# Optimization experiments

Measured on AMD Instinct MI355X. Metric: run time of the kernel, lower is better.

## Reference

```python
import jax, jax.numpy as jnp
import numpy as np

HIDDEN = 1024
HEADS = 16
DEPTH = HIDDEN // HEADS  # 64
B, F, T = 2, 2048, 2048


def setup_inputs() -> dict:
    key = jax.random.key(0)
    ks = jax.random.split(key, 7)
    return {
        "query_input": jax.random.normal(ks[0], (B, F, HIDDEN), dtype=jnp.float32),
        "source_input": jax.random.normal(ks[1], (B, T, HIDDEN), dtype=jnp.float32),
        "bias": jax.random.normal(ks[2], (1, 1, F, T), dtype=jnp.float32),
        "wq": jax.random.normal(ks[3], (HIDDEN, HEADS, DEPTH), dtype=jnp.float32) * 0.02,
        "wk": jax.random.normal(ks[4], (HIDDEN, HEADS, DEPTH), dtype=jnp.float32) * 0.02,
        "wv": jax.random.normal(ks[5], (HIDDEN, HEADS, DEPTH), dtype=jnp.float32) * 0.02,
        "wo": jax.random.normal(ks[6], (HEADS, DEPTH, HIDDEN), dtype=jnp.float32) * 0.02,
    }


def reference(query_input, source_input, bias, wq, wk, wv, wo):
    # projections: [B,S,C] x [C,N,H] -> [B,S,N,H]
    q = jnp.einsum("bfc,cnh->bfnh", query_input, wq)
    k = jnp.einsum("btc,cnh->btnh", source_input, wk)
    v = jnp.einsum("btc,cnh->btnh", source_input, wv)
    q = q * (DEPTH ** -0.5)
    # logits: [B,N,F,T], softmax over T (last dim)
    logits = jnp.einsum("btnh,bfnh->bnft", k, q)
    logits = logits + bias
    weights = jax.nn.softmax(logits, axis=3)
    attn = jnp.einsum("bnft,btnh->bfnh", weights, v)
    out = jnp.einsum("bfnh,nhe->bfe", attn, wo)
    return out
```

## Files before the change

kernel.cpp:

```cpp
#include <hip/hip_runtime.h>

#define LOG2E 1.44269504f

typedef __attribute__((ext_vector_type(8))) short short8v;
typedef __attribute__((ext_vector_type(4))) float f32x4;
typedef unsigned int u32;
typedef __attribute__((address_space(1))) const u32* gp_t;
typedef __attribute__((address_space(3))) u32* lp_t;

#define MFMA(a, b, c) __builtin_amdgcn_mfma_f32_16x16x32_bf16((a), (b), (c), 0, 0, 0)

__device__ __forceinline__ unsigned short f2bf(float f) {
  unsigned int u = __float_as_uint(f);
  u = (u + 0x7fffu + ((u >> 16) & 1u)) >> 16;
  return (unsigned short)u;
}
__device__ __forceinline__ u32 cvtpk(float lo, float hi) {
  u32 r;
  asm("v_cvt_pk_bf16_f32 %0, %1, %2" : "=v"(r) : "v"(lo), "v"(hi));
  return r;
}

__global__ void k_cvt2(const float* __restrict__ a, const float* __restrict__ bsrc,
                       unsigned short* __restrict__ oa, unsigned short* __restrict__ ob,
                       int n4each) {
  int stride = gridDim.x * blockDim.x;
  for (int i = blockIdx.x * blockDim.x + threadIdx.x; i < 2 * n4each; i += stride) {
    bool second = i >= n4each;
    int j = second ? i - n4each : i;
    float4 v = second ? reinterpret_cast<const float4*>(bsrc)[j]
                      : reinterpret_cast<const float4*>(a)[j];
    ushort4 o;
    o.x = f2bf(v.x); o.y = f2bf(v.y); o.z = f2bf(v.z); o.w = f2bf(v.w);
    (second ? reinterpret_cast<ushort4*>(ob) : reinterpret_cast<ushort4*>(oa))[j] = o;
  }
}

__global__ void k_cvt_t4(const float* __restrict__ w0, const float* __restrict__ w1,
                         const float* __restrict__ w2, const float* __restrict__ w3,
                         unsigned short* __restrict__ wqkvT, unsigned short* __restrict__ woT) {
  __shared__ float tile[32][33];
  int z = blockIdx.z;
  const float* in = (z == 0) ? w0 : (z == 1) ? w1 : (z == 2) ? w2 : w3;
  unsigned short* out = (z < 3) ? (wqkvT + (size_t)z * 1048576) : woT;
  float scale = (z == 0) ? 0.125f * LOG2E : 1.0f;
  int bx = blockIdx.x * 32, by = blockIdx.y * 32;
  int tx = threadIdx.x, ty = threadIdx.y;
  for (int r = ty; r < 32; r += 8)
    tile[r][tx] = in[(size_t)(by + r) * 1024 + bx + tx];
  __syncthreads();
  for (int r = ty; r < 32; r += 8)
    out[(size_t)(bx + r) * 1024 + by + tx] = f2bf(tile[tx][r] * scale);
}

__global__ void k_bias_perm(const float* __restrict__ in, float* __restrict__ out) {
  int bid = blockIdx.x;
  int fb = bid >> 5, ch = bid & 31;
  int tid = threadIdx.x;
  int tt = tid >> 6, rem = tid & 63;
  int g = rem >> 4, l15 = rem & 15;
  float4 v = *reinterpret_cast<const float4*>(
      &in[(size_t)(fb * 16 + l15) * 2048 + ch * 64 + tt * 16 + g * 4]);
  v.x *= LOG2E; v.y *= LOG2E; v.z *= LOG2E; v.w *= LOG2E;
  *reinterpret_cast<float4*>(&out[(size_t)bid * 1024 + tid * 4]) = v;
}

__global__ __launch_bounds__(256)
void k_gemmqkv(const unsigned short* __restrict__ Aq, const unsigned short* __restrict__ Asrc,
               const unsigned short* __restrict__ W,
               unsigned short* __restrict__ dq, unsigned short* __restrict__ dk,
               unsigned short* __restrict__ dv) {
  __shared__ __align__(16) unsigned short Al[2][8192];
  __shared__ __align__(16) unsigned short Bl[2][4096];
  const int tid = threadIdx.x;
  const int lane = tid & 63, wid = tid >> 6;
  const int g = lane >> 4, l15 = lane & 15, l7 = l15 & 7;
  const int wm = wid >> 1, wn = wid & 1;
  const int rowbase = blockIdx.y * 128;
  const int colbase = blockIdx.x * 64;
  const bool isV = colbase >= 2048;
  const unsigned short* A = (colbase < 1024) ? Aq : Asrc;
  const int xgl = (g ^ l7) << 4;

  const int jr = tid >> 3;
  const int sc = ((tid & 7) ^ (jr & 7)) << 3;
  const unsigned short* As0 = A + (size_t)(rowbase + jr) * 1024 + sc;
  const unsigned short* Ws0 = W + (size_t)(colbase + jr) * 1024 + sc;

  const f32x4 zf = {0.f, 0.f, 0.f, 0.f};
  f32x4 acc[4][2];
#pragma unroll
  for (int mf = 0; mf < 4; ++mf) { acc[mf][0] = zf; acc[mf][1] = zf; }

  auto stage = [&](int buf, int k0) {
    char* Ad = (char*)&Al[buf][0];
    char* Bd = (char*)&Bl[buf][0];
#pragma unroll
    for (int p = 0; p < 4; ++p)
      __builtin_amdgcn_global_load_lds((gp_t)(As0 + (size_t)p * 32 * 1024 + k0),
                                       (lp_t)(Ad + (p * 256 + tid) * 16), 16, 0, 0);
#pragma unroll
    for (int p = 0; p < 2; ++p)
      __builtin_amdgcn_global_load_lds((gp_t)(Ws0 + (size_t)p * 32 * 1024 + k0),
                                       (lp_t)(Bd + (p * 256 + tid) * 16), 16, 0, 0);
  };
  auto ldfrags = [&](int buf, int kk, short8v af[4], short8v bfr[2]) {
    const char* Ac = (const char*)&Al[buf][0];
    const char* Bc = (const char*)&Bl[buf][0];
#pragma unroll
    for (int mf = 0; mf < 4; ++mf)
      af[mf] = *reinterpret_cast<const short8v*>(
          Ac + ((wm * 64 + mf * 16 + l15) << 7) + (xgl ^ (kk << 6)));
#pragma unroll
    for (int nf = 0; nf < 2; ++nf)
      bfr[nf] = *reinterpret_cast<const short8v*>(
          Bc + ((wn * 32 + nf * 16 + l15) << 7) + (xgl ^ (kk << 6)));
  };

  stage(0, 0);
  __syncthreads();
#pragma unroll 1
  for (int s = 0; s < 16; ++s) {
    if (s < 15) stage((s + 1) & 1, (s + 1) * 64);
    __builtin_amdgcn_s_setprio(1);
    if (!isV) {
#pragma unroll
      for (int kk = 0; kk < 2; ++kk) {
        short8v af[4], bfr[2];
        ldfrags(s & 1, kk, af, bfr);
#pragma unroll
        for (int mf = 0; mf < 4; ++mf)
#pragma unroll
          for (int nf = 0; nf < 2; ++nf) acc[mf][nf] = MFMA(bfr[nf], af[mf], acc[mf][nf]);
      }
    } else {
#pragma unroll
      for (int kk = 0; kk < 2; ++kk) {
        short8v af[4], bfr[2];
        ldfrags(s & 1, kk, af, bfr);
#pragma unroll
        for (int mf = 0; mf < 4; ++mf)
#pragma unroll
          for (int nf = 0; nf < 2; ++nf) acc[mf][nf] = MFMA(af[mf], bfr[nf], acc[mf][nf]);
      }
    }
    __builtin_amdgcn_s_setprio(0);
    __syncthreads();
  }

  if (!isV) {
    unsigned short* dst = (colbase < 1024) ? dq : dk;
    const int cb = colbase & 1023;
#pragma unroll
    for (int mf = 0; mf < 4; ++mf)
#pragma unroll
      for (int nf = 0; nf < 2; ++nf) {
        f32x4 v = acc[mf][nf];
        int s = rowbase + wm * 64 + mf * 16 + l15;
        int c = cb + wn * 32 + nf * 16 + g * 4;
        int b = s >> 11, s2 = s & 2047, hd = c >> 6, h = c & 63;
        uint2 w; w.x = cvtpk(v[0], v[1]); w.y = cvtpk(v[2], v[3]);
        *reinterpret_cast<uint2*>(dst + ((size_t)(b * 16 + hd) * 2048 + s2) * 64 + h) = w;
      }
  } else {
    const int cb = colbase - 2048;
#pragma unroll
    for (int mf = 0; mf < 4; ++mf)
#pragma unroll
      for (int nf = 0; nf < 2; ++nf) {
        f32x4 v = acc[mf][nf];
        int s = rowbase + wm * 64 + mf * 16 + g * 4;
        int c = cb + wn * 32 + nf * 16 + l15;
        int b = s >> 11, s2 = s & 2047, hd = c >> 6, h = c & 63;
        uint2 w; w.x = cvtpk(v[0], v[1]); w.y = cvtpk(v[2], v[3]);
        *reinterpret_cast<uint2*>(dv + ((size_t)(b * 16 + hd) * 64 + h) * 2048 + s2) = w;
      }
  }
}

template <int TC, int MODE>
__global__ __launch_bounds__(256, 4)
void k_gemm(const unsigned short* __restrict__ A, const unsigned short* __restrict__ BT,
            void* __restrict__ dstv) {
  __shared__ __align__(16) unsigned short Al[2][4096];
  __shared__ __align__(16) unsigned short Bl[2][4096];
  const int tid = threadIdx.x;
  const int lane = tid & 63, wid = tid >> 6;
  const int g = lane >> 4, l15 = lane & 15, l7 = l15 & 7;
  const int wm = wid >> 1, wn = wid & 1;
  const int rowbase = blockIdx.y * 64, colbase = blockIdx.x * 64;
  const int xgl = (g ^ l7) << 4;

  const int jr = tid >> 3;
  const int sc = ((tid & 7) ^ (jr & 7)) << 3;
  const unsigned short* As0 = A + (size_t)(rowbase + jr) * 1024 + sc;
  const unsigned short* As1 = A + (size_t)(rowbase + jr + 32) * 1024 + sc;
  const unsigned short* Bs0 = BT + (size_t)(colbase + jr) * 1024 + sc;
  const unsigned short* Bs1 = BT + (size_t)(colbase + jr + 32) * 1024 + sc;

  const f32x4 zf = {0.f, 0.f, 0.f, 0.f};
  f32x4 acc[2][2];
  acc[0][0] = zf; acc[0][1] = zf; acc[1][0] = zf; acc[1][1] = zf;

  auto stage = [&](int buf, int k0) {
    char* Ad = (char*)&Al[buf][0];
    char* Bd = (char*)&Bl[buf][0];
    __builtin_amdgcn_global_load_lds((gp_t)(As0 + k0), (lp_t)(Ad + tid * 16), 16, 0, 0);
    __builtin_amdgcn_global_load_lds((gp_t)(As1 + k0), (lp_t)(Ad + 4096 + tid * 16), 16, 0, 0);
    __builtin_amdgcn_global_load_lds((gp_t)(Bs0 + k0), (lp_t)(Bd + tid * 16), 16, 0, 0);
    __builtin_amdgcn_global_load_lds((gp_t)(Bs1 + k0), (lp_t)(Bd + 4096 + tid * 16), 16, 0, 0);
  };
  auto compute = [&](int buf) {
    const char* Ac = (const char*)&Al[buf][0];
    const char* Bc = (const char*)&Bl[buf][0];
    __builtin_amdgcn_s_setprio(1);
#pragma unroll
    for (int kk = 0; kk < 2; ++kk) {
      short8v af[2], bfr[2];
#pragma unroll
      for (int mf = 0; mf < 2; ++mf)
        af[mf] = *reinterpret_cast<const short8v*>(
            Ac + ((wm * 32 + mf * 16 + l15) << 7) + (xgl ^ (kk << 6)));
#pragma unroll
      for (int nf = 0; nf < 2; ++nf)
        bfr[nf] = *reinterpret_cast<const short8v*>(
            Bc + ((wn * 32 + nf * 16 + l15) << 7) + (xgl ^ (kk << 6)));
#pragma unroll
      for (int mf = 0; mf < 2; ++mf)
#pragma unroll
        for (int nf = 0; nf < 2; ++nf)
          acc[mf][nf] = TC ? MFMA(bfr[nf], af[mf], acc[mf][nf])
                           : MFMA(af[mf], bfr[nf], acc[mf][nf]);
    }
    __builtin_amdgcn_s_setprio(0);
  };

  stage(0, 0);
  __syncthreads();
#pragma unroll 1
  for (int s = 0; s < 16; ++s) {
    if (s < 15) stage((s + 1) & 1, (s + 1) * 64);
    compute(s & 1);
    __syncthreads();
  }

#pragma unroll
  for (int mf = 0; mf < 2; ++mf)
#pragma unroll
    for (int nf = 0; nf < 2; ++nf) {
      f32x4 v = acc[mf][nf];
      if (MODE == 2) {
        int s = rowbase + wm * 32 + mf * 16 + l15;
        int c = colbase + wn * 32 + nf * 16 + g * 4;
        *reinterpret_cast<f32x4*>((float*)dstv + (size_t)s * 1024 + c) = v;
      }
    }
}

__global__ __launch_bounds__(256, 4)
void k_attn(const unsigned short* __restrict__ qw,
            const unsigned short* __restrict__ kw,
            const unsigned short* __restrict__ vtw,
            const float* __restrict__ biaspf,
            unsigned short* __restrict__ attnb) {
  __shared__ __align__(16) unsigned short Kl[2][4096];
  __shared__ __align__(16) unsigned short Vl[2][4096];
  __shared__ __align__(16) unsigned short Pl[4][1024];

  const int tid = threadIdx.x;
  const int lane = tid & 63, wid = tid >> 6;
  const int g = lane >> 4, l15 = lane & 15, l7 = l15 & 7;
  const int xgl = (g ^ l7) << 4;

  const int bid = blockIdx.x;
  const int ft = bid >> 5, bn = bid & 31;
  const int b = bn >> 4, n = bn & 15;

  const size_t hoff = (size_t)bn * (2048 * 64);
  const unsigned short* qp = qw + hoff;
  const unsigned short* kp = kw + hoff;
  const unsigned short* vp = vtw + hoff;

  const int f0 = ft * 64 + wid * 16;
  const int fb = ft * 4 + wid;

  const int jr = tid >> 3;
  const int sc = ((tid & 7) ^ (jr & 7)) << 3;
  const unsigned short* Ks0 = kp + jr * 64 + sc;
  const unsigned short* Ks1 = kp + (jr + 32) * 64 + sc;
  const unsigned short* Vs0 = vp + jr * 2048 + sc;
  const unsigned short* Vs1 = vp + (jr + 32) * 2048 + sc;
  char* K0d = (char*)&Kl[0][0]; char* K1d = (char*)&Kl[1][0];
  char* V0d = (char*)&Vl[0][0]; char* V1d = (char*)&Vl[1][0];

  auto stage = [&](char* Kd, char* Vd, int ci) {
    int ko = ci << 12, vo = ci << 6;
    __builtin_amdgcn_global_load_lds((gp_t)(Ks0 + ko), (lp_t)(Kd + tid * 16), 16, 0, 0);
    __builtin_amdgcn_global_load_lds((gp_t)(Ks1 + ko), (lp_t)(Kd + 4096 + tid * 16), 16, 0, 0);
    __builtin_amdgcn_global_load_lds((gp_t)(Vs0 + vo), (lp_t)(Vd + tid * 16), 16, 0, 0);
    __builtin_amdgcn_global_load_lds((gp_t)(Vs1 + vo), (lp_t)(Vd + 4096 + tid * 16), 16, 0, 0);
  };

  short8v aq0 = *reinterpret_cast<const short8v*>(&qp[(size_t)(f0 + l15) * 64 + g * 8]);
  short8v aq1 = *reinterpret_cast<const short8v*>(&qp[(size_t)(f0 + l15) * 64 + 32 + g * 8]);

  const float* bias_lane = biaspf + (size_t)fb * 32768 + lane * 4;

  const f32x4 zf = {0.f, 0.f, 0.f, 0.f};
  f32x4 o[4];
  o[0] = zf; o[1] = zf; o[2] = zf; o[3] = zf;
  float ls = 0.f;
  char* Pbl = (char*)&Pl[wid][0] + l15 * 128;

  auto bload = [&](int ci, f32x4* bc) {
#pragma unroll
    for (int tt = 0; tt < 4; ++tt)
      bc[tt] = *reinterpret_cast<const f32x4*>(bias_lane + ci * 1024 + tt * 256);
  };

  auto compute = [&](const unsigned short* Kb, const unsigned short* Vb, const f32x4* bc) {
    const char* Kc = (const char*)Kb; const char* Vc = (const char*)Vb;
    f32x4 st[4];
    __builtin_amdgcn_s_setprio(1);
#pragma unroll
    for (int tt = 0; tt < 4; ++tt) {
      short8v kb0 = *reinterpret_cast<const short8v*>(Kc + ((tt * 16 + l15) << 7) + xgl);
      short8v kb1 = *reinterpret_cast<const short8v*>(Kc + ((tt * 16 + l15) << 7) + (xgl ^ 64));
      st[tt] = MFMA(kb1, aq1, MFMA(kb0, aq0, bc[tt]));
    }
    __builtin_amdgcn_s_setprio(0);

    float rs = 0.f;
#pragma unroll
    for (int tt = 0; tt < 4; ++tt) {
      float p0 = __builtin_amdgcn_exp2f(st[tt][0]);
      float p1 = __builtin_amdgcn_exp2f(st[tt][1]);
      float p2 = __builtin_amdgcn_exp2f(st[tt][2]);
      float p3 = __builtin_amdgcn_exp2f(st[tt][3]);
      rs += (p0 + p1) + (p2 + p3);
      uint2 w;
      w.x = cvtpk(p0, p1);
      w.y = cvtpk(p2, p3);
      *reinterpret_cast<uint2*>(Pbl + ((tt * 32 + g * 8) ^ (l7 * 16))) = w;
    }
    rs += __shfl_xor(rs, 16);
    rs += __shfl_xor(rs, 32);
    ls += rs;

    __builtin_amdgcn_s_setprio(1);
#pragma unroll
    for (int c = 0; c < 2; ++c) {
      short8v pa = *reinterpret_cast<const short8v*>(Pbl + ((c << 6) ^ xgl));
#pragma unroll
      for (int ht = 0; ht < 4; ++ht) {
        short8v vb = *reinterpret_cast<const short8v*>(
            Vc + ((ht * 16 + l15) << 7) + (xgl ^ (c << 6)));
        o[ht] = MFMA(pa, vb, o[ht]);
      }
    }
    __builtin_amdgcn_s_setprio(0);
  };

  f32x4 cb[4], nb[4];
  stage(K0d, V0d, 0);
  bload(0, cb);
  __syncthreads();
#pragma unroll 1
  for (int ci = 0; ci < 32; ci += 2) {
    stage(K1d, V1d, (ci + 1) & 31);
    bload((ci + 1) & 31, nb);
    compute(Kl[0], Vl[0], cb);
#pragma unroll
    for (int q = 0; q < 4; ++q) cb[q] = nb[q];
    __syncthreads();
    stage(K0d, V0d, (ci + 2) & 31);
    bload((ci + 2) & 31, nb);
    compute(Kl[1], Vl[1], cb);
#pragma unroll
    for (int q = 0; q < 4; ++q) cb[q] = nb[q];
    __syncthreads();
  }

  float inv = 1.f / ls;
  float i0 = __shfl(inv, g * 4 + 0, 16);
  float i1 = __shfl(inv, g * 4 + 1, 16);
  float i2 = __shfl(inv, g * 4 + 2, 16);
  float i3 = __shfl(inv, g * 4 + 3, 16);
#pragma unroll
  for (int ht = 0; ht < 4; ++ht) {
    unsigned short* ob = &attnb[((size_t)b * 2048 + f0 + g * 4) * 1024 + n * 64 + ht * 16 + l15];
    ob[0] = f2bf(o[ht][0] * i0);
    ob[1024] = f2bf(o[ht][1] * i1);
    ob[2048] = f2bf(o[ht][2] * i2);
    ob[3072] = f2bf(o[ht][3] * i3);
  }
}

extern "C" void kernel_launch(void* const* d_in, const int* in_sizes, int n_in,
                              void* d_out, int out_size, void* d_ws, size_t ws_size,
                              hipStream_t stream) {
  const float* query  = (const float*)d_in[0];
  const float* source = (const float*)d_in[1];
  const float* bias   = (const float*)d_in[2];
  const float* wq     = (const float*)d_in[3];
  const float* wk     = (const float*)d_in[4];
  const float* wv     = (const float*)d_in[5];
  const float* wo     = (const float*)d_in[6];

  char* ws = (char*)d_ws;
  unsigned short* qin_b  = (unsigned short*)(ws + 0);
  unsigned short* src_b  = (unsigned short*)(ws + 8388608);
  float*          bias_f = (float*)(ws + 0);
  unsigned short* wqkvT  = (unsigned short*)(ws + 16777216);
  unsigned short* woT    = (unsigned short*)(ws + 23068672);
  unsigned short* q_ws   = (unsigned short*)(ws + 25165824);
  unsigned short* k_ws   = (unsigned short*)(ws + 33554432);
  unsigned short* vT_ws  = (unsigned short*)(ws + 41943040);
  unsigned short* attn_b = (unsigned short*)(ws + 50331648);

  k_cvt2<<<2048, 256, 0, stream>>>(query, source, qin_b, src_b, 1048576);
  dim3 tb(32, 8);
  k_cvt_t4<<<dim3(32, 32, 4), tb, 0, stream>>>(wq, wk, wv, wo, wqkvT, woT);

  k_gemmqkv<<<dim3(48, 32), 256, 0, stream>>>(qin_b, src_b, wqkvT, q_ws, k_ws, vT_ws);
  k_bias_perm<<<4096, 256, 0, stream>>>(bias, bias_f);
  k_attn<<<1024, 256, 0, stream>>>(q_ws, k_ws, vT_ws, bias_f, attn_b);
  k_gemm<1, 2><<<dim3(16, 64), 256, 0, stream>>>(attn_b, woT, d_out);
}
```

Baseline: 143.8 us.

## Double rows per wave in attention and enlarge output GEMM tile

```diff
diff --git a/kernel.cpp b/kernel.cpp
--- a/kernel.cpp
+++ b/kernel.cpp
@@ -178,61 +178,40 @@
   }
 }
 
-template <int TC, int MODE>
-__global__ __launch_bounds__(256, 4)
-void k_gemm(const unsigned short* __restrict__ A, const unsigned short* __restrict__ BT,
-            void* __restrict__ dstv) {
-  __shared__ __align__(16) unsigned short Al[2][4096];
+__global__ __launch_bounds__(256)
+void k_gemmo(const unsigned short* __restrict__ A, const unsigned short* __restrict__ W,
+             float* __restrict__ df) {
+  __shared__ __align__(16) unsigned short Al[2][8192];
   __shared__ __align__(16) unsigned short Bl[2][4096];
   const int tid = threadIdx.x;
   const int lane = tid & 63, wid = tid >> 6;
   const int g = lane >> 4, l15 = lane & 15, l7 = l15 & 7;
   const int wm = wid >> 1, wn = wid & 1;
-  const int rowbase = blockIdx.y * 64, colbase = blockIdx.x * 64;
+  const int rowbase = blockIdx.y * 128;
+  const int colbase = blockIdx.x * 64;
   const int xgl = (g ^ l7) << 4;
 
   const int jr = tid >> 3;
   const int sc = ((tid & 7) ^ (jr & 7)) << 3;
   const unsigned short* As0 = A + (size_t)(rowbase + jr) * 1024 + sc;
-  const unsigned short* As1 = A + (size_t)(rowbase + jr + 32) * 1024 + sc;
-  const unsigned short* Bs0 = BT + (size_t)(colbase + jr) * 1024 + sc;
-  const unsigned short* Bs1 = BT + (size_t)(colbase + jr + 32) * 1024 + sc;
+  const unsigned short* Ws0 = W + (size_t)(colbase + jr) * 1024 + sc;
 
   const f32x4 zf = {0.f, 0.f, 0.f, 0.f};
-  f32x4 acc[2][2];
-  acc[0][0] = zf; acc[0][1] = zf; acc[1][0] = zf; acc[1][1] = zf;
+  f32x4 acc[4][2];
+#pragma unroll
+  for (int mf = 0; mf < 4; ++mf) { acc[mf][0] = zf; acc[mf][1] = zf; }
 
   auto stage = [&](int buf, int k0) {
     char* Ad = (char*)&Al[buf][0];
     char* Bd = (char*)&Bl[buf][0];
-    __builtin_amdgcn_global_load_lds((gp_t)(As0 + k0), (lp_t)(Ad + tid * 16), 16, 0, 0);
-    __builtin_amdgcn_global_load_lds((gp_t)(As1 + k0), (lp_t)(Ad + 4096 + tid * 16), 16, 0, 0);
-    __builtin_amdgcn_global_load_lds((gp_t)(Bs0 + k0), (lp_t)(Bd + tid * 16), 16, 0, 0);
-    __builtin_amdgcn_global_load_lds((gp_t)(Bs1 + k0), (lp_t)(Bd + 4096 + tid * 16), 16, 0, 0);
-  };
-  auto compute = [&](int buf) {
-    const char* Ac = (const char*)&Al[buf][0];
-    const char* Bc = (const char*)&Bl[buf][0];
-    __builtin_amdgcn_s_setprio(1);
-#pragma unroll
-    for (int kk = 0; kk < 2; ++kk) {
-      short8v af[2], bfr[2];
-#pragma unroll
-      for (int mf = 0; mf < 2; ++mf)
-        af[mf] = *reinterpret_cast<const short8v*>(
-            Ac + ((wm * 32 + mf * 16 + l15) << 7) + (xgl ^ (kk << 6)));
-#pragma unroll
-      for (int nf = 0; nf < 2; ++nf)
-        bfr[nf] = *reinterpret_cast<const short8v*>(
-            Bc + ((wn * 32 + nf * 16 + l15) << 7) + (xgl ^ (kk << 6)));
-#pragma unroll
-      for (int mf = 0; mf < 2; ++mf)
-#pragma unroll
-        for (int nf = 0; nf < 2; ++nf)
-          acc[mf][nf] = TC ? MFMA(bfr[nf], af[mf], acc[mf][nf])
-                           : MFMA(af[mf], bfr[nf], acc[mf][nf]);
-    }
-    __builtin_amdgcn_s_setprio(0);
+#pragma unroll
+    for (int p = 0; p < 4; ++p)
+      __builtin_amdgcn_global_load_lds((gp_t)(As0 + (size_t)p * 32 * 1024 + k0),
+                                       (lp_t)(Ad + (p * 256 + tid) * 16), 16, 0, 0);
+#pragma unroll
+    for (int p = 0; p < 2; ++p)
+      __builtin_amdgcn_global_load_lds((gp_t)(Ws0 + (size_t)p * 32 * 1024 + k0),
+                                       (lp_t)(Bd + (p * 256 + tid) * 16), 16, 0, 0);
   };
 
   stage(0, 0);
@@ -240,24 +219,40 @@
 #pragma unroll 1
   for (int s = 0; s < 16; ++s) {
     if (s < 15) stage((s + 1) & 1, (s + 1) * 64);
-    compute(s & 1);
+    const char* Ac = (const char*)&Al[s & 1][0];
+    const char* Bc = (const char*)&Bl[s & 1][0];
+    __builtin_amdgcn_s_setprio(1);
+#pragma unroll
+    for (int kk = 0; kk < 2; ++kk) {
+      short8v af[4], bfr[2];
+#pragma unroll
+      for (int mf = 0; mf < 4; ++mf)
+        af[mf] = *reinterpret_cast<const short8v*>(
+            Ac + ((wm * 64 + mf * 16 + l15) << 7) + (xgl ^ (kk << 6)));
+#pragma unroll
+      for (int nf = 0; nf < 2; ++nf)
+        bfr[nf] = *reinterpret_cast<const short8v*>(
+            Bc + ((wn * 32 + nf * 16 + l15) << 7) + (xgl ^ (kk << 6)));
+#pragma unroll
+      for (int mf = 0; mf < 4; ++mf)
+#pragma unroll
+        for (int nf = 0; nf < 2; ++nf) acc[mf][nf] = MFMA(bfr[nf], af[mf], acc[mf][nf]);
+    }
+    __builtin_amdgcn_s_setprio(0);
     __syncthreads();
   }
 
 #pragma unroll
-  for (int mf = 0; mf < 2; ++mf)
+  for (int mf = 0; mf < 4; ++mf)
 #pragma unroll
     for (int nf = 0; nf < 2; ++nf) {
-      f32x4 v = acc[mf][nf];
-      if (MODE == 2) {
-        int s = rowbase + wm * 32 + mf * 16 + l15;
-        int c = colbase + wn * 32 + nf * 16 + g * 4;
-        *reinterpret_cast<f32x4*>((float*)dstv + (size_t)s * 1024 + c) = v;
-      }
-    }
-}
-
-__global__ __launch_bounds__(256, 4)
+      int s = rowbase + wm * 64 + mf * 16 + l15;
+      int c = colbase + wn * 32 + nf * 16 + g * 4;
+      *reinterpret_cast<f32x4*>(df + (size_t)s * 1024 + c) = acc[mf][nf];
+    }
+}
+
+__global__ __launch_bounds__(256, 2)
 void k_attn(const unsigned short* __restrict__ qw,
             const unsigned short* __restrict__ kw,
             const unsigned short* __restrict__ vtw,
@@ -265,7 +260,7 @@
             unsigned short* __restrict__ attnb) {
   __shared__ __align__(16) unsigned short Kl[2][4096];
   __shared__ __align__(16) unsigned short Vl[2][4096];
-  __shared__ __align__(16) unsigned short Pl[4][1024];
+  __shared__ __align__(16) unsigned short Pl[4][2048];
 
   const int tid = threadIdx.x;
   const int lane = tid & 63, wid = tid >> 6;
@@ -281,8 +276,8 @@
   const unsigned short* kp = kw + hoff;
   const unsigned short* vp = vtw + hoff;
 
-  const int f0 = ft * 64 + wid * 16;
-  const int fb = ft * 4 + wid;
+  const int f0 = ft * 128 + wid * 32;
+  const int fbb = ft * 8 + wid * 2;
 
   const int jr = tid >> 3;
   const int sc = ((tid & 7) ^ (jr & 7)) << 3;
@@ -301,67 +296,86 @@
     __builtin_amdgcn_global_load_lds((gp_t)(Vs1 + vo), (lp_t)(Vd + 4096 + tid * 16), 16, 0, 0);
   };
 
-  short8v aq0 = *reinterpret_cast<const short8v*>(&qp[(size_t)(f0 + l15) * 64 + g * 8]);
-  short8v aq1 = *reinterpret_cast<const short8v*>(&qp[(size_t)(f0 + l15) * 64 + 32 + g * 8]);
-
-  const float* bias_lane = biaspf + (size_t)fb * 32768 + lane * 4;
+  short8v aq[2][2];
+#pragma unroll
+  for (int rg = 0; rg < 2; ++rg) {
+    aq[rg][0] = *reinterpret_cast<const short8v*>(
+        &qp[(size_t)(f0 + rg * 16 + l15) * 64 + g * 8]);
+    aq[rg][1] = *reinterpret_cast<const short8v*>(
+        &qp[(size_t)(f0 + rg * 16 + l15) * 64 + 32 + g * 8]);
+  }
+
+  const float* bias_lane = biaspf + (size_t)fbb * 32768 + lane * 4;
 
   const f32x4 zf = {0.f, 0.f, 0.f, 0.f};
-  f32x4 o[4];
-  o[0] = zf; o[1] = zf; o[2] = zf; o[3] = zf;
-  float ls = 0.f;
-  char* Pbl = (char*)&Pl[wid][0] + l15 * 128;
-
-  auto bload = [&](int ci, f32x4* bc) {
-#pragma unroll
-    for (int tt = 0; tt < 4; ++tt)
-      bc[tt] = *reinterpret_cast<const f32x4*>(bias_lane + ci * 1024 + tt * 256);
-  };
-
-  auto compute = [&](const unsigned short* Kb, const unsigned short* Vb, const f32x4* bc) {
+  f32x4 o[2][4];
+#pragma unroll
+  for (int rg = 0; rg < 2; ++rg)
+#pragma unroll
+    for (int ht = 0; ht < 4; ++ht) o[rg][ht] = zf;
+  float ls0 = 0.f, ls1 = 0.f;
+  char* Pb = (char*)&Pl[wid][0] + l15 * 128;
+
+  auto bload = [&](int ci, f32x4 bc[2][4]) {
+#pragma unroll
+    for (int rg = 0; rg < 2; ++rg)
+#pragma unroll
+      for (int tt = 0; tt < 4; ++tt)
+        bc[rg][tt] = *reinterpret_cast<const f32x4*>(
+            bias_lane + (size_t)rg * 32768 + ci * 1024 + tt * 256);
+  };
+
+  auto compute = [&](const unsigned short* Kb, const unsigned short* Vb,
+                     const f32x4 bc[2][4]) {
     const char* Kc = (const char*)Kb; const char* Vc = (const char*)Vb;
-    f32x4 st[4];
+    f32x4 st[2][4];
     __builtin_amdgcn_s_setprio(1);
 #pragma unroll
     for (int tt = 0; tt < 4; ++tt) {
       short8v kb0 = *reinterpret_cast<const short8v*>(Kc + ((tt * 16 + l15) << 7) + xgl);
       short8v kb1 = *reinterpret_cast<const short8v*>(Kc + ((tt * 16 + l15) << 7) + (xgl ^ 64));
-      st[tt] = MFMA(kb1, aq1, MFMA(kb0, aq0, bc[tt]));
+      st[0][tt] = MFMA(kb1, aq[0][1], MFMA(kb0, aq[0][0], bc[0][tt]));
+      st[1][tt] = MFMA(kb1, aq[1][1], MFMA(kb0, aq[1][0], bc[1][tt]));
     }
     __builtin_amdgcn_s_setprio(0);
 
-    float rs = 0.f;
-#pragma unroll
-    for (int tt = 0; tt < 4; ++tt) {
-      float p0 = __builtin_amdgcn_exp2f(st[tt][0]);
-      float p1 = __builtin_amdgcn_exp2f(st[tt][1]);
-      float p2 = __builtin_amdgcn_exp2f(st[tt][2]);
-      float p3 = __builtin_amdgcn_exp2f(st[tt][3]);
-      rs += (p0 + p1) + (p2 + p3);
-      uint2 w;
-      w.x = cvtpk(p0, p1);
-      w.y = cvtpk(p2, p3);
-      *reinterpret_cast<uint2*>(Pbl + ((tt * 32 + g * 8) ^ (l7 * 16))) = w;
-    }
-    rs += __shfl_xor(rs, 16);
-    rs += __shfl_xor(rs, 32);
-    ls += rs;
+#pragma unroll
+    for (int rg = 0; rg < 2; ++rg) {
+      float rs = 0.f;
+#pragma unroll
+      for (int tt = 0; tt < 4; ++tt) {
+        float p0 = __builtin_amdgcn_exp2f(st[rg][tt][0]);
+        float p1 = __builtin_amdgcn_exp2f(st[rg][tt][1]);
+        float p2 = __builtin_amdgcn_exp2f(st[rg][tt][2]);
+        float p3 = __builtin_amdgcn_exp2f(st[rg][tt][3]);
+        rs += (p0 + p1) + (p2 + p3);
+        uint2 w;
+        w.x = cvtpk(p0, p1);
+        w.y = cvtpk(p2, p3);
+        *reinterpret_cast<uint2*>(Pb + rg * 2048 + ((tt * 32 + g * 8) ^ (l7 * 16))) = w;
+      }
+      rs += __shfl_xor(rs, 16);
+      rs += __shfl_xor(rs, 32);
+      if (rg == 0) ls0 += rs; else ls1 += rs;
+    }
 
     __builtin_amdgcn_s_setprio(1);
 #pragma unroll
     for (int c = 0; c < 2; ++c) {
-      short8v pa = *reinterpret_cast<const short8v*>(Pbl + ((c << 6) ^ xgl));
+      short8v pa0 = *reinterpret_cast<const short8v*>(Pb + ((c << 6) ^ xgl));
+      short8v pa1 = *reinterpret_cast<const short8v*>(Pb + 2048 + ((c << 6) ^ xgl));
 #pragma unroll
       for (int ht = 0; ht < 4; ++ht) {
         short8v vb = *reinterpret_cast<const short8v*>(
             Vc + ((ht * 16 + l15) << 7) + (xgl ^ (c << 6)));
-        o[ht] = MFMA(pa, vb, o[ht]);
+        o[0][ht] = MFMA(pa0, vb, o[0][ht]);
+        o[1][ht] = MFMA(pa1, vb, o[1][ht]);
       }
     }
     __builtin_amdgcn_s_setprio(0);
   };
 
-  f32x4 cb[4], nb[4];
+  f32x4 cb[2][4], nb[2][4];
   stage(K0d, V0d, 0);
   bload(0, cb);
   __syncthreads();
@@ -371,28 +385,36 @@
     bload((ci + 1) & 31, nb);
     compute(Kl[0], Vl[0], cb);
 #pragma unroll
-    for (int q = 0; q < 4; ++q) cb[q] = nb[q];
+    for (int rg = 0; rg < 2; ++rg)
+#pragma unroll
+      for (int q = 0; q < 4; ++q) cb[rg][q] = nb[rg][q];
     __syncthreads();
     stage(K0d, V0d, (ci + 2) & 31);
     bload((ci + 2) & 31, nb);
     compute(Kl[1], Vl[1], cb);
 #pragma unroll
-    for (int q = 0; q < 4; ++q) cb[q] = nb[q];
+    for (int rg = 0; rg < 2; ++rg)
+#pragma unroll
+      for (int q = 0; q < 4; ++q) cb[rg][q] = nb[rg][q];
     __syncthreads();
   }
 
-  float inv = 1.f / ls;
-  float i0 = __shfl(inv, g * 4 + 0, 16);
-  float i1 = __shfl(inv, g * 4 + 1, 16);
-  float i2 = __shfl(inv, g * 4 + 2, 16);
-  float i3 = __shfl(inv, g * 4 + 3, 16);
-#pragma unroll
-  for (int ht = 0; ht < 4; ++ht) {
-    unsigned short* ob = &attnb[((size_t)b * 2048 + f0 + g * 4) * 1024 + n * 64 + ht * 16 + l15];
-    ob[0] = f2bf(o[ht][0] * i0);
-    ob[1024] = f2bf(o[ht][1] * i1);
-    ob[2048] = f2bf(o[ht][2] * i2);
-    ob[3072] = f2bf(o[ht][3] * i3);
+#pragma unroll
+  for (int rg = 0; rg < 2; ++rg) {
+    float inv = 1.f / (rg == 0 ? ls0 : ls1);
+    float i0 = __shfl(inv, g * 4 + 0, 16);
+    float i1 = __shfl(inv, g * 4 + 1, 16);
+    float i2 = __shfl(inv, g * 4 + 2, 16);
+    float i3 = __shfl(inv, g * 4 + 3, 16);
+#pragma unroll
+    for (int ht = 0; ht < 4; ++ht) {
+      unsigned short* ob = &attnb[((size_t)b * 2048 + f0 + rg * 16 + g * 4) * 1024 +
+                                  n * 64 + ht * 16 + l15];
+      ob[0] = f2bf(o[rg][ht][0] * i0);
+      ob[1024] = f2bf(o[rg][ht][1] * i1);
+      ob[2048] = f2bf(o[rg][ht][2] * i2);
+      ob[3072] = f2bf(o[rg][ht][3] * i3);
+    }
   }
 }
 
@@ -424,6 +446,6 @@
 
   k_gemmqkv<<<dim3(48, 32), 256, 0, stream>>>(qin_b, src_b, wqkvT, q_ws, k_ws, vT_ws);
   k_bias_perm<<<4096, 256, 0, stream>>>(bias, bias_f);
-  k_attn<<<1024, 256, 0, stream>>>(q_ws, k_ws, vT_ws, bias_f, attn_b);
-  k_gemm<1, 2><<<dim3(16, 64), 256, 0, stream>>>(attn_b, woT, d_out);
-}
+  k_attn<<<512, 256, 0, stream>>>(q_ws, k_ws, vT_ws, bias_f, attn_b);
+  k_gemmo<<<dim3(16, 32), 256, 0, stream>>>(attn_b, woT, (float*)d_out);
+}
```

Result: faster. 138.6 us (-3.6%).
